# Kernel tuning notes

Measured on AMD Instinct MI355X. Metric: run time of the kernel, lower is better.

Reference implementation:

```python
import jax, jax.numpy as jnp
import numpy as np

INPUT_DIM = 512
HIDDEN_DIM = 1024
OUTPUT_DIM = 512
SEQ_LEN = 16384


def setup_inputs() -> dict:
    key = jax.random.key(0)
    ks = jax.random.split(key, 8)
    s = 1.0 / np.sqrt(HIDDEN_DIM)
    X = jax.random.normal(ks[0], (SEQ_LEN, INPUT_DIM), dtype=jnp.float32)
    # PyTorch GRU params: weight_ih [3H, D], weight_hh [3H, H], biases [3H]; gate order r, z, n
    W_ih = jax.random.uniform(ks[1], (3 * HIDDEN_DIM, INPUT_DIM), minval=-s, maxval=s, dtype=jnp.float32)
    W_hh = jax.random.uniform(ks[2], (3 * HIDDEN_DIM, HIDDEN_DIM), minval=-s, maxval=s, dtype=jnp.float32)
    b_ih = jax.random.uniform(ks[3], (3 * HIDDEN_DIM,), minval=-s, maxval=s, dtype=jnp.float32)
    b_hh = jax.random.uniform(ks[4], (3 * HIDDEN_DIM,), minval=-s, maxval=s, dtype=jnp.float32)
    W_fc = jax.random.uniform(ks[5], (OUTPUT_DIM, HIDDEN_DIM), minval=-s, maxval=s, dtype=jnp.float32)
    b_fc = jax.random.uniform(ks[6], (OUTPUT_DIM,), minval=-s, maxval=s, dtype=jnp.float32)
    return {"X": X, "W_ih": W_ih, "W_hh": W_hh, "b_ih": b_ih, "b_hh": b_hh, "W_fc": W_fc, "b_fc": b_fc}


def _gru_seq(X, W_ih, W_hh, b_ih, b_hh):
    H = W_hh.shape[1]
    # Precompute input projections for all timesteps in one GEMM: [T, 3H]
    gx = X @ W_ih.T + b_ih

    def step(h, gx_t):
        gxr, gxz, gxn = gx_t[:H], gx_t[H:2 * H], gx_t[2 * H:]
        gh = h @ W_hh.T + b_hh
        ghr, ghz, ghn = gh[:H], gh[H:2 * H], gh[2 * H:]
        r = jax.nn.sigmoid(gxr + ghr)
        z = jax.nn.sigmoid(gxz + ghz)
        n = jnp.tanh(gxn + r * ghn)
        h_new = (1.0 - z) * n + z * h
        return h_new, h_new

    h0 = jnp.zeros((H,), dtype=X.dtype)
    _, hs = jax.lax.scan(step, h0, gx)  # hs: [T, H]
    return hs


def reference(X, W_ih, W_hh, b_ih, b_hh, W_fc, b_fc):
    hs = _gru_seq(X, W_ih, W_hh, b_ih, b_hh)  # [T, H]
    return hs @ W_fc.T + b_fc  # [T, output_dim]
```

## Files before the change

### kernel.cpp

```cpp
#include <hip/hip_runtime.h>
#include <hip/hip_bf16.h>

#define H      1024
#define IN_DIM 512
#define OD     512
#define T_LEN  16384
#define NWG    256
#define NREP   16
#define RS     (H + 64)
#define PSTRIDE (NREP * RS)

typedef unsigned long long u64;
typedef unsigned int u32;

__device__ __forceinline__ u32 pack_bf(float lo, float hi) {
    u32 a = __float_as_uint(lo); a = (a + 0x7fffu + ((a >> 16) & 1u)) >> 16;
    u32 b = __float_as_uint(hi); b = (b + 0x7fffu + ((b >> 16) & 1u)) & 0xffff0000u;
    return a | b;
}
__device__ __forceinline__ float bf_lo(u32 pk) { return __uint_as_float(pk << 16); }
__device__ __forceinline__ float bf_hi(u32 pk) { return __uint_as_float(pk & 0xffff0000u); }

__global__ __launch_bounds__(256, 1)
void gru_rec_kernel(const float* __restrict__ X,
                    const float* __restrict__ Wih,
                    const float* __restrict__ Whh,
                    const float* __restrict__ bih,
                    const float* __restrict__ bhh,
                    float* __restrict__ hs,
                    u32* __restrict__ vals)
{
    __shared__ u64 lsh[2][8][64];

    const int tid  = threadIdx.x;
    const int wave = tid >> 6;
    const int lane = tid & 63;
    const int wg   = blockIdx.x;
    const int gw   = wg * 4 + wave;
    const int u    = gw;

    u32 whh_r[3][8];
    u32 wih_r[3][4];
    #pragma unroll
    for (int g = 0; g < 3; ++g) {
        const float* wr = Whh + (size_t)(g * H + u) * H;
        #pragma unroll
        for (int k = 0; k < 8; ++k)
            whh_r[g][k] = pack_bf(wr[2 * lane + 128 * k], wr[2 * lane + 1 + 128 * k]);
        const float* wx = Wih + (size_t)(g * H + u) * IN_DIM;
        #pragma unroll
        for (int k = 0; k < 4; ++k)
            wih_r[g][k] = pack_bf(wx[2 * lane + 128 * k], wx[2 * lane + 1 + 128 * k]);
    }
    const float bxr = bih[u], bxz = bih[H + u], bxn = bih[2 * H + u];
    const float bhr = bhh[u], bhz = bhh[H + u], bhn = bhh[2 * H + u];

    {
        u32* lp = (u32*)lsh;
        for (int i = tid; i < 2048; i += 256) lp[i] = (i < 1024) ? 0u : 1u;
    }
    __syncthreads();

    float xw[8];
    #pragma unroll
    for (int k = 0; k < 4; ++k) {
        float2 vv = *(const float2*)(X + 2 * lane + 128 * k);
        xw[2 * k] = vv.x; xw[2 * k + 1] = vv.y;
    }
    float pxr = 0.f, pxz = 0.f, pxns = 0.f;
    {
        float xn = 0.f;
        #pragma unroll
        for (int k = 0; k < 4; ++k) {
            const float x0 = xw[2 * k], x1 = xw[2 * k + 1];
            pxr += bf_lo(wih_r[0][k]) * x0 + bf_hi(wih_r[0][k]) * x1;
            pxz += bf_lo(wih_r[1][k]) * x0 + bf_hi(wih_r[1][k]) * x1;
            xn  += bf_lo(wih_r[2][k]) * x0 + bf_hi(wih_r[2][k]) * x1;
        }
        #pragma unroll
        for (int s = 32; s; s >>= 1) xn += __shfl_xor(xn, s, 64);
        pxns = xn;
    }

    const int rep = wg & (NREP - 1);
    float hmine = 0.f;

    #pragma unroll 1
    for (int t = 0; t < T_LEN; ++t) {
        const u32 lapexp = (u32)((t >> 1) & 1);
        const int p = t & 1;
        u64 v[8];

        if (wave == 0) {
            const u64* pb = (const u64*)(vals + (size_t)p * PSTRIDE
                                              + (size_t)rep * RS) + lane;
            for (;;) {
                #pragma unroll
                for (int k = 0; k < 8; ++k)
                    v[k] = __hip_atomic_load(pb + 64 * k, __ATOMIC_RELAXED,
                                             __HIP_MEMORY_SCOPE_AGENT);
                u32 bad = 0;
                #pragma unroll
                for (int k = 0; k < 8; ++k)
                    bad |= ((u32)v[k] ^ lapexp) | ((u32)(v[k] >> 32) ^ lapexp);
                if (!(bad & 1u)) break;
            }
            #pragma unroll
            for (int k = 0; k < 8; ++k)
                __hip_atomic_store(&lsh[p][k][lane], v[k], __ATOMIC_RELAXED,
                                   __HIP_MEMORY_SCOPE_WORKGROUP);
        } else {
            for (;;) {
                u32 bad = 0;
                #pragma unroll
                for (int k = 0; k < 8; ++k) {
                    v[k] = __hip_atomic_load(&lsh[p][k][lane], __ATOMIC_RELAXED,
                                             __HIP_MEMORY_SCOPE_WORKGROUP);
                    bad |= ((u32)v[k] ^ lapexp) | ((u32)(v[k] >> 32) ^ lapexp);
                }
                if (!(bad & 1u)) break;
            }
        }

        if (t && wave == 1 && wg == ((t - 1) & 255)) {
            u64* dst = (u64*)(hs + (size_t)(t - 1) * H) + lane;
            #pragma unroll
            for (int k = 0; k < 8; ++k) dst[64 * k] = v[k];
        }

        float xn2[8];
        {
            const int tn = (t + 1 < T_LEN) ? (t + 1) : t;
            const float* xp = X + (size_t)tn * IN_DIM;
            #pragma unroll
            for (int k = 0; k < 4; ++k) {
                float2 vv = *(const float2*)(xp + 2 * lane + 128 * k);
                xn2[2 * k] = vv.x; xn2[2 * k + 1] = vv.y;
            }
        }

        float ar = pxr, az = pxz, anh = 0.f;
        #pragma unroll
        for (int k = 0; k < 8; ++k) {
            const float h0 = __uint_as_float((u32)v[k]);
            const float h1 = __uint_as_float((u32)(v[k] >> 32));
            ar  += bf_lo(whh_r[0][k]) * h0 + bf_hi(whh_r[0][k]) * h1;
            az  += bf_lo(whh_r[1][k]) * h0 + bf_hi(whh_r[1][k]) * h1;
            anh += bf_lo(whh_r[2][k]) * h0 + bf_hi(whh_r[2][k]) * h1;
        }
        #pragma unroll
        for (int s = 32; s; s >>= 1) {
            ar  += __shfl_xor(ar,  s, 64);
            az  += __shfl_xor(az,  s, 64);
            anh += __shfl_xor(anh, s, 64);
        }

        const float r = 1.f / (1.f + __expf(-(ar + bxr + bhr)));
        const float z = 1.f / (1.f + __expf(-(az + bxz + bhz)));
        const float e2 = __expf(2.f * (pxns + bxn + r * (anh + bhn)));
        const float n = 1.f - 2.f / (e2 + 1.f);
        const float hnew = (1.f - z) * n + z * hmine;
        const u32 lapw = (u32)(((t + 1) >> 1) & 1);
        const u32 bits = (__float_as_uint(hnew) & ~1u) | lapw;
        hmine = __uint_as_float(bits);
        if (lane < NREP)
            __hip_atomic_store(vals + (size_t)((t + 1) & 1) * PSTRIDE
                                    + (size_t)lane * RS + u,
                               bits, __ATOMIC_RELAXED, __HIP_MEMORY_SCOPE_AGENT);
        if (t == T_LEN - 1 && lane == 0)
            hs[(size_t)t * H + u] = hmine;

        {
            float xr2 = 0.f, xz2 = 0.f, xn3 = 0.f;
            #pragma unroll
            for (int k = 0; k < 4; ++k) {
                const float x0 = xn2[2 * k], x1 = xn2[2 * k + 1];
                xr2 += bf_lo(wih_r[0][k]) * x0 + bf_hi(wih_r[0][k]) * x1;
                xz2 += bf_lo(wih_r[1][k]) * x0 + bf_hi(wih_r[1][k]) * x1;
                xn3 += bf_lo(wih_r[2][k]) * x0 + bf_hi(wih_r[2][k]) * x1;
            }
            #pragma unroll
            for (int s = 32; s; s >>= 1) xn3 += __shfl_xor(xn3, s, 64);
            pxr = xr2; pxz = xz2; pxns = xn3;
        }
    }
}

#define BM 64
#define BN 64
#define BK 16
__global__ __launch_bounds__(256)
void fc_kernel(const float* __restrict__ A, const float* __restrict__ B,
               const float* __restrict__ bias, float* __restrict__ C)
{
    __shared__ float As[BK][BM + 4];
    __shared__ float Bs[BK][BN + 4];
    const int tid = threadIdx.x;
    const int m0 = blockIdx.y * BM, n0 = blockIdx.x * BN;
    const int tx = tid & 15, ty = tid >> 4;
    float acc[4][4] = {};
    const int r = tid >> 2, c = (tid & 3) << 2;
    for (int k0 = 0; k0 < H; k0 += BK) {
        float4 va = *(const float4*)(A + (size_t)(m0 + r) * H + (k0 + c));
        As[c + 0][r] = va.x; As[c + 1][r] = va.y; As[c + 2][r] = va.z; As[c + 3][r] = va.w;
        float4 vb = *(const float4*)(B + (size_t)(n0 + r) * H + (k0 + c));
        Bs[c + 0][r] = vb.x; Bs[c + 1][r] = vb.y; Bs[c + 2][r] = vb.z; Bs[c + 3][r] = vb.w;
        __syncthreads();
        #pragma unroll
        for (int kk = 0; kk < BK; ++kk) {
            float4 a4 = *(const float4*)&As[kk][ty * 4];
            float4 b4 = *(const float4*)&Bs[kk][tx * 4];
            const float av[4] = {a4.x, a4.y, a4.z, a4.w};
            const float bv[4] = {b4.x, b4.y, b4.z, b4.w};
            #pragma unroll
            for (int i = 0; i < 4; ++i)
                #pragma unroll
                for (int j = 0; j < 4; ++j)
                    acc[i][j] += av[i] * bv[j];
        }
        __syncthreads();
    }
    #pragma unroll
    for (int i = 0; i < 4; ++i) {
        const int m = m0 + ty * 4 + i;
        #pragma unroll
        for (int j = 0; j < 4; ++j) {
            const int n = n0 + tx * 4 + j;
            C[(size_t)m * OD + n] = acc[i][j] + bias[n];
        }
    }
}

extern "C" void kernel_launch(void* const* d_in, const int* in_sizes, int n_in,
                              void* d_out, int out_size, void* d_ws, size_t ws_size,
                              hipStream_t stream) {
    const float* X   = (const float*)d_in[0];
    const float* Wih = (const float*)d_in[1];
    const float* Whh = (const float*)d_in[2];
    const float* bih = (const float*)d_in[3];
    const float* bhh = (const float*)d_in[4];
    const float* Wfc = (const float*)d_in[5];
    const float* bfc = (const float*)d_in[6];
    float* out = (float*)d_out;

    float* hs  = (float*)d_ws;
    u32*  vals = (u32*)((char*)d_ws + (size_t)T_LEN * H * 4);

    hipMemsetAsync(vals, 0x00, (size_t)PSTRIDE * 4, stream);
    hipMemsetAsync(vals + PSTRIDE, 0x01, (size_t)PSTRIDE * 4, stream);

    void* args[] = { (void*)&X, (void*)&Wih, (void*)&Whh, (void*)&bih,
                     (void*)&bhh, (void*)&hs, (void*)&vals };
    hipError_t e = hipLaunchCooperativeKernel((const void*)gru_rec_kernel,
                                              dim3(NWG), dim3(256), args, 0, stream);
    if (e != hipSuccess) {
        gru_rec_kernel<<<dim3(NWG), dim3(256), 0, stream>>>(X, Wih, Whh, bih, bhh, hs, vals);
    }

    dim3 fgrid(OD / BN, T_LEN / BM);
    fc_kernel<<<fgrid, dim3(256), 0, stream>>>(hs, Wfc, bfc, out);
}
```

Measured before the change: 28.74 ms.

## Give each wave two hidden units and shrink the recurrent grid to 64 workgroups

The persistent GRU recurrence kernel now launches 64 workgroups of 512 threads instead of 256 workgroups of 256 threads. Each wave computes two hidden units, publishing both as one packed 64-bit atomic store. The number of h-state replicas drops from 16 to 8. The aim is to cut the number of workgroups polling global memory at each timestep, and with it the cross-workgroup sync cost. The trade-off is roughly double the register pressure and per-wave compute on the serial critical path, with fewer CUs in use.

```diff
diff --git a/kernel.cpp b/kernel.cpp
--- a/kernel.cpp
+++ b/kernel.cpp
@@ -5,8 +5,8 @@
 #define IN_DIM 512
 #define OD     512
 #define T_LEN  16384
-#define NWG    256
-#define NREP   16
+#define NWG    64
+#define NREP   8
 #define RS     (H + 64)
 #define PSTRIDE (NREP * RS)
 
@@ -21,7 +21,7 @@
 __device__ __forceinline__ float bf_lo(u32 pk) { return __uint_as_float(pk << 16); }
 __device__ __forceinline__ float bf_hi(u32 pk) { return __uint_as_float(pk & 0xffff0000u); }
 
-__global__ __launch_bounds__(256, 1)
+__global__ __launch_bounds__(512, 2)
 void gru_rec_kernel(const float* __restrict__ X,
                     const float* __restrict__ Wih,
                     const float* __restrict__ Whh,
@@ -36,28 +36,33 @@
     const int wave = tid >> 6;
     const int lane = tid & 63;
     const int wg   = blockIdx.x;
-    const int gw   = wg * 4 + wave;
-    const int u    = gw;
-
-    u32 whh_r[3][8];
-    u32 wih_r[3][4];
+    const int gw   = wg * 8 + wave;
+    const int u0   = 2 * gw, u1 = 2 * gw + 1;
+
+    u32 whh_r[6][8];
+    u32 wih_r[6][4];
     #pragma unroll
     for (int g = 0; g < 3; ++g) {
-        const float* wr = Whh + (size_t)(g * H + u) * H;
-        #pragma unroll
-        for (int k = 0; k < 8; ++k)
-            whh_r[g][k] = pack_bf(wr[2 * lane + 128 * k], wr[2 * lane + 1 + 128 * k]);
-        const float* wx = Wih + (size_t)(g * H + u) * IN_DIM;
-        #pragma unroll
-        for (int k = 0; k < 4; ++k)
-            wih_r[g][k] = pack_bf(wx[2 * lane + 128 * k], wx[2 * lane + 1 + 128 * k]);
-    }
-    const float bxr = bih[u], bxz = bih[H + u], bxn = bih[2 * H + u];
-    const float bhr = bhh[u], bhz = bhh[H + u], bhn = bhh[2 * H + u];
+        #pragma unroll
+        for (int j = 0; j < 2; ++j) {
+            const float* wr = Whh + (size_t)(g * H + 2 * gw + j) * H;
+            #pragma unroll
+            for (int k = 0; k < 8; ++k)
+                whh_r[g * 2 + j][k] = pack_bf(wr[2 * lane + 128 * k], wr[2 * lane + 1 + 128 * k]);
+            const float* wx = Wih + (size_t)(g * H + 2 * gw + j) * IN_DIM;
+            #pragma unroll
+            for (int k = 0; k < 4; ++k)
+                wih_r[g * 2 + j][k] = pack_bf(wx[2 * lane + 128 * k], wx[2 * lane + 1 + 128 * k]);
+        }
+    }
+    const float bxr0 = bih[u0], bxz0 = bih[H + u0], bxn0 = bih[2 * H + u0];
+    const float bhr0 = bhh[u0], bhz0 = bhh[H + u0], bhn0 = bhh[2 * H + u0];
+    const float bxr1 = bih[u1], bxz1 = bih[H + u1], bxn1 = bih[2 * H + u1];
+    const float bhr1 = bhh[u1], bhz1 = bhh[H + u1], bhn1 = bhh[2 * H + u1];
 
     {
         u32* lp = (u32*)lsh;
-        for (int i = tid; i < 2048; i += 256) lp[i] = (i < 1024) ? 0u : 1u;
+        for (int i = tid; i < 2048; i += 512) lp[i] = (i < 1024) ? 0u : 1u;
     }
     __syncthreads();
 
@@ -67,23 +72,29 @@
         float2 vv = *(const float2*)(X + 2 * lane + 128 * k);
         xw[2 * k] = vv.x; xw[2 * k + 1] = vv.y;
     }
-    float pxr = 0.f, pxz = 0.f, pxns = 0.f;
+    float pxr0 = 0.f, pxr1 = 0.f, pxz0 = 0.f, pxz1 = 0.f, pxn0 = 0.f, pxn1 = 0.f;
     {
-        float xn = 0.f;
+        float n0 = 0.f, n1 = 0.f;
         #pragma unroll
         for (int k = 0; k < 4; ++k) {
             const float x0 = xw[2 * k], x1 = xw[2 * k + 1];
-            pxr += bf_lo(wih_r[0][k]) * x0 + bf_hi(wih_r[0][k]) * x1;
-            pxz += bf_lo(wih_r[1][k]) * x0 + bf_hi(wih_r[1][k]) * x1;
-            xn  += bf_lo(wih_r[2][k]) * x0 + bf_hi(wih_r[2][k]) * x1;
-        }
-        #pragma unroll
-        for (int s = 32; s; s >>= 1) xn += __shfl_xor(xn, s, 64);
-        pxns = xn;
+            pxr0 += bf_lo(wih_r[0][k]) * x0 + bf_hi(wih_r[0][k]) * x1;
+            pxr1 += bf_lo(wih_r[1][k]) * x0 + bf_hi(wih_r[1][k]) * x1;
+            pxz0 += bf_lo(wih_r[2][k]) * x0 + bf_hi(wih_r[2][k]) * x1;
+            pxz1 += bf_lo(wih_r[3][k]) * x0 + bf_hi(wih_r[3][k]) * x1;
+            n0   += bf_lo(wih_r[4][k]) * x0 + bf_hi(wih_r[4][k]) * x1;
+            n1   += bf_lo(wih_r[5][k]) * x0 + bf_hi(wih_r[5][k]) * x1;
+        }
+        #pragma unroll
+        for (int s = 32; s; s >>= 1) {
+            n0 += __shfl_xor(n0, s, 64);
+            n1 += __shfl_xor(n1, s, 64);
+        }
+        pxn0 = n0; pxn1 = n1;
     }
 
     const int rep = wg & (NREP - 1);
-    float hmine = 0.f;
+    float hmine0 = 0.f, hmine1 = 0.f;
 
     #pragma unroll 1
     for (int t = 0; t < T_LEN; ++t) {
@@ -122,7 +133,7 @@
             }
         }
 
-        if (t && wave == 1 && wg == ((t - 1) & 255)) {
+        if (t && wave == 1 && wg == ((t - 1) & (NWG - 1))) {
             u64* dst = (u64*)(hs + (size_t)(t - 1) * H) + lane;
             #pragma unroll
             for (int k = 0; k < 8; ++k) dst[64 * k] = v[k];
@@ -139,49 +150,72 @@
             }
         }
 
-        float ar = pxr, az = pxz, anh = 0.f;
+        float a0 = pxr0, a1 = pxr1, a2 = pxz0, a3 = pxz1, a4 = 0.f, a5 = 0.f;
         #pragma unroll
         for (int k = 0; k < 8; ++k) {
             const float h0 = __uint_as_float((u32)v[k]);
             const float h1 = __uint_as_float((u32)(v[k] >> 32));
-            ar  += bf_lo(whh_r[0][k]) * h0 + bf_hi(whh_r[0][k]) * h1;
-            az  += bf_lo(whh_r[1][k]) * h0 + bf_hi(whh_r[1][k]) * h1;
-            anh += bf_lo(whh_r[2][k]) * h0 + bf_hi(whh_r[2][k]) * h1;
+            a0 += bf_lo(whh_r[0][k]) * h0 + bf_hi(whh_r[0][k]) * h1;
+            a1 += bf_lo(whh_r[1][k]) * h0 + bf_hi(whh_r[1][k]) * h1;
+            a2 += bf_lo(whh_r[2][k]) * h0 + bf_hi(whh_r[2][k]) * h1;
+            a3 += bf_lo(whh_r[3][k]) * h0 + bf_hi(whh_r[3][k]) * h1;
+            a4 += bf_lo(whh_r[4][k]) * h0 + bf_hi(whh_r[4][k]) * h1;
+            a5 += bf_lo(whh_r[5][k]) * h0 + bf_hi(whh_r[5][k]) * h1;
         }
         #pragma unroll
         for (int s = 32; s; s >>= 1) {
-            ar  += __shfl_xor(ar,  s, 64);
-            az  += __shfl_xor(az,  s, 64);
-            anh += __shfl_xor(anh, s, 64);
-        }
-
-        const float r = 1.f / (1.f + __expf(-(ar + bxr + bhr)));
-        const float z = 1.f / (1.f + __expf(-(az + bxz + bhz)));
-        const float e2 = __expf(2.f * (pxns + bxn + r * (anh + bhn)));
-        const float n = 1.f - 2.f / (e2 + 1.f);
-        const float hnew = (1.f - z) * n + z * hmine;
+            a0 += __shfl_xor(a0, s, 64);
+            a1 += __shfl_xor(a1, s, 64);
+            a2 += __shfl_xor(a2, s, 64);
+            a3 += __shfl_xor(a3, s, 64);
+            a4 += __shfl_xor(a4, s, 64);
+            a5 += __shfl_xor(a5, s, 64);
+        }
+
+        const float r0 = 1.f / (1.f + __expf(-(a0 + bxr0 + bhr0)));
+        const float z0 = 1.f / (1.f + __expf(-(a2 + bxz0 + bhz0)));
+        const float e0 = __expf(2.f * (pxn0 + bxn0 + r0 * (a4 + bhn0)));
+        const float n0 = 1.f - 2.f / (e0 + 1.f);
+        const float h0 = (1.f - z0) * n0 + z0 * hmine0;
+
+        const float r1 = 1.f / (1.f + __expf(-(a1 + bxr1 + bhr1)));
+        const float z1 = 1.f / (1.f + __expf(-(a3 + bxz1 + bhz1)));
+        const float e1 = __expf(2.f * (pxn1 + bxn1 + r1 * (a5 + bhn1)));
+        const float n1 = 1.f - 2.f / (e1 + 1.f);
+        const float h1 = (1.f - z1) * n1 + z1 * hmine1;
+
         const u32 lapw = (u32)(((t + 1) >> 1) & 1);
-        const u32 bits = (__float_as_uint(hnew) & ~1u) | lapw;
-        hmine = __uint_as_float(bits);
+        const u32 bits0 = (__float_as_uint(h0) & ~1u) | lapw;
+        const u32 bits1 = (__float_as_uint(h1) & ~1u) | lapw;
+        hmine0 = __uint_as_float(bits0);
+        hmine1 = __uint_as_float(bits1);
+        const u64 pk = ((u64)bits1 << 32) | (u64)bits0;
         if (lane < NREP)
-            __hip_atomic_store(vals + (size_t)((t + 1) & 1) * PSTRIDE
-                                    + (size_t)lane * RS + u,
-                               bits, __ATOMIC_RELAXED, __HIP_MEMORY_SCOPE_AGENT);
+            __hip_atomic_store((u64*)(vals + (size_t)((t + 1) & 1) * PSTRIDE
+                                           + (size_t)lane * RS) + gw,
+                               pk, __ATOMIC_RELAXED, __HIP_MEMORY_SCOPE_AGENT);
+
         if (t == T_LEN - 1 && lane == 0)
-            hs[(size_t)t * H + u] = hmine;
+            ((u64*)(hs + (size_t)t * H))[gw] = pk;
 
         {
-            float xr2 = 0.f, xz2 = 0.f, xn3 = 0.f;
+            float xr0 = 0.f, xr1 = 0.f, xz0 = 0.f, xz1 = 0.f, n0e = 0.f, n1e = 0.f;
             #pragma unroll
             for (int k = 0; k < 4; ++k) {
                 const float x0 = xn2[2 * k], x1 = xn2[2 * k + 1];
-                xr2 += bf_lo(wih_r[0][k]) * x0 + bf_hi(wih_r[0][k]) * x1;
-                xz2 += bf_lo(wih_r[1][k]) * x0 + bf_hi(wih_r[1][k]) * x1;
-                xn3 += bf_lo(wih_r[2][k]) * x0 + bf_hi(wih_r[2][k]) * x1;
-            }
-            #pragma unroll
-            for (int s = 32; s; s >>= 1) xn3 += __shfl_xor(xn3, s, 64);
-            pxr = xr2; pxz = xz2; pxns = xn3;
+                xr0 += bf_lo(wih_r[0][k]) * x0 + bf_hi(wih_r[0][k]) * x1;
+                xr1 += bf_lo(wih_r[1][k]) * x0 + bf_hi(wih_r[1][k]) * x1;
+                xz0 += bf_lo(wih_r[2][k]) * x0 + bf_hi(wih_r[2][k]) * x1;
+                xz1 += bf_lo(wih_r[3][k]) * x0 + bf_hi(wih_r[3][k]) * x1;
+                n0e += bf_lo(wih_r[4][k]) * x0 + bf_hi(wih_r[4][k]) * x1;
+                n1e += bf_lo(wih_r[5][k]) * x0 + bf_hi(wih_r[5][k]) * x1;
+            }
+            #pragma unroll
+            for (int s = 32; s; s >>= 1) {
+                n0e += __shfl_xor(n0e, s, 64);
+                n1e += __shfl_xor(n1e, s, 64);
+            }
+            pxr0 = xr0; pxr1 = xr1; pxz0 = xz0; pxz1 = xz1; pxn0 = n0e; pxn1 = n1e;
         }
     }
 }
@@ -252,9 +286,9 @@
     void* args[] = { (void*)&X, (void*)&Wih, (void*)&Whh, (void*)&bih,
                      (void*)&bhh, (void*)&hs, (void*)&vals };
     hipError_t e = hipLaunchCooperativeKernel((const void*)gru_rec_kernel,
-                                              dim3(NWG), dim3(256), args, 0, stream);
+                                              dim3(NWG), dim3(512), args, 0, stream);
     if (e != hipSuccess) {
-        gru_rec_kernel<<<dim3(NWG), dim3(256), 0, stream>>>(X, Wih, Whh, bih, bhh, hs, vals);
+        gru_rec_kernel<<<dim3(NWG), dim3(512), 0, stream>>>(X, Wih, Whh, bih, bhh, hs, vals);
     }
 
     dim3 fgrid(OD / BN, T_LEN / BM);
```

Result: slower. 35.38 ms (+23.1%).
